# Optimization experiments

Measured on AMD Instinct MI355X. Metric: run time of the kernel, lower is better.

The kernel has to match this reference:

```python
import jax, jax.numpy as jnp
import numpy as np

N_NODES = 100000
N_EDGES = 1600000
D = 128
LAYERS = 3
LN_EPS = 1e-5


def setup_inputs() -> dict:
    key = jax.random.key(0)
    k1, k2, k3 = jax.random.split(key, 3)
    x = jax.random.normal(k1, (N_NODES, D), dtype=jnp.float32)
    edge_index = jax.random.randint(k2, (2, N_EDGES), 0, N_NODES, dtype=jnp.int64)
    W = jax.random.normal(k3, (LAYERS, D, D), dtype=jnp.float32) * (1.0 / np.sqrt(D))
    b = jnp.zeros((LAYERS, D), dtype=jnp.float32)
    ln_w = jnp.ones((LAYERS, D), dtype=jnp.float32)
    ln_b = jnp.zeros((LAYERS, D), dtype=jnp.float32)
    return {"x": x, "edge_index": edge_index, "W": W, "b": b, "ln_w": ln_w, "ln_b": ln_b}


def _gcn_conv(x, row, col, deg_inv_sqrt, W, b):
    # x: [N, D]; row/col: [E+N] (self-loops appended); PyG GCNConv math:
    # h = (D^-1/2 (A+I) D^-1/2) (x @ W) + b
    xw = x @ W  # [N, D]
    norm = deg_inv_sqrt[row] * deg_inv_sqrt[col]  # [E+N]
    msg = xw[row] * norm[:, None]  # gather + scale, memory-bound
    out = jax.ops.segment_sum(msg, col, num_segments=x.shape[0])  # scatter-add at targets
    return out + b


def _layer_norm(h, w, bset):
    mu = jnp.mean(h, axis=-1, keepdims=True)
    var = jnp.mean(jnp.square(h - mu), axis=-1, keepdims=True)
    return (h - mu) * jax.lax.rsqrt(var + LN_EPS) * w + bset


def reference(x, edge_index, W, b, ln_w, ln_b):
    n = x.shape[0]
    loops = jnp.arange(n, dtype=edge_index.dtype)
    row = jnp.concatenate([edge_index[0], loops])  # sources
    col = jnpp = jnp.concatenate([edge_index[1], loops])  # targets
    deg = jax.ops.segment_sum(jnp.ones_like(col, dtype=x.dtype), col, num_segments=n)
    deg_inv_sqrt = jax.lax.rsqrt(deg)  # deg >= 1 due to self-loops
    for i in range(LAYERS):
        h = _gcn_conv(x, row, col, deg_inv_sqrt, W[i], b[i])
        h = jax.nn.relu(h)
        h = h + x  # residual (shapes always match: in == emb)
        # dropout is identity in eval mode
        x = _layer_norm(h, ln_w[i], ln_b[i])
    return x
```

## Files before the change

kernel.cpp:

```cpp
#include <hip/hip_runtime.h>
#include <stdint.h>

#define NN 100000
#define NE 1600000
#define DD 128
#define NLAYERS 3
#define NB 196
#define BRS 9
#define NBLK 256
#define EPB 6250
#define CAP 96
#define ENTCAP 9216
#define OVFCAP 4096

typedef __attribute__((ext_vector_type(8))) short bf16x8;
typedef __attribute__((ext_vector_type(4))) float f32x4;
typedef __attribute__((ext_vector_type(4))) unsigned int u32x4;
typedef __attribute__((ext_vector_type(2))) unsigned int u32x2;
typedef __attribute__((ext_vector_type(2))) float f32x2;

__device__ __forceinline__ float bflo(uint32_t v){ return __uint_as_float(v << 16); }
__device__ __forceinline__ float bfhi(uint32_t v){ return __uint_as_float(v & 0xFFFF0000u); }
__device__ __forceinline__ float bf1(unsigned short u){ return __uint_as_float(((uint32_t)u) << 16); }
__device__ __forceinline__ unsigned short f2bf(float f){
  uint32_t u = __float_as_uint(f);
  u += 0x7FFFu + ((u >> 16) & 1u);
  return (unsigned short)(u >> 16);
}
__device__ __forceinline__ int colof(int j){ return ((j & 7) << 4) | (j >> 3); }

__global__ __launch_bounds__(256) void k_detect(const uint32_t* __restrict__ x,
                                                const uint32_t* __restrict__ ei,
                                                int* __restrict__ flags){
  __shared__ int s_f32, s_i32;
  if (threadIdx.x == 0){ s_f32 = 0; s_i32 = 0; }
  __syncthreads();
  int f = 0, i32 = 0;
  for (int idx = threadIdx.x; idx < 8192; idx += 256){
    uint32_t u = x[idx];
    if (((u >> 7) & 0xFFu) >= 0x90u) f++;
  }
  for (int idx = threadIdx.x; idx < 2048; idx += 256){
    if (ei[2*idx + 1] != 0u) i32++;
  }
  atomicAdd(&s_f32, f); atomicAdd(&s_i32, i32);
  __syncthreads();
  if (threadIdx.x == 0){
    flags[0] = (s_f32 > 100) ? 1 : 0;
    flags[1] = (s_i32 > 10) ? 0 : 1;
  }
}

__device__ __forceinline__ int load_edge(const int* ei, int i64m, size_t idx){
  if (i64m) return (int)((const uint32_t*)ei)[2*idx];
  return ei[idx];
}


__global__ __launch_bounds__(256) void k_params(const void* __restrict__ W, const void* __restrict__ b,
                                                const void* __restrict__ lnw, const void* __restrict__ lnb,
                                                const int* __restrict__ flags,
                                                unsigned short* __restrict__ wt,
                                                float* __restrict__ pbP, float* __restrict__ plwP,
                                                float* __restrict__ plbP){
  int l = blockIdx.x;
  int f32m = flags[0];
  for (int idx = threadIdx.x; idx < DD*DD; idx += 256){
    int k = idx >> 7, c = idx & 127;
    unsigned short v = f32m ? f2bf(((const float*)W)[l*DD*DD + idx])
                            : ((const unsigned short*)W)[l*DD*DD + idx];
    wt[l*DD*DD + c*DD + k] = v;
  }
  for (int idx = threadIdx.x; idx < DD; idx += 256){
    int c = colof(idx);
    if (f32m){
      pbP [l*DD+idx] = ((const float*)b)[l*DD+c];
      plwP[l*DD+idx] = ((const float*)lnw)[l*DD+c];
      plbP[l*DD+idx] = ((const float*)lnb)[l*DD+c];
    } else {
      pbP [l*DD+idx] = bf1(((const unsigned short*)b)[l*DD+c]);
      plwP[l*DD+idx] = bf1(((const unsigned short*)lnw)[l*DD+c]);
      plbP[l*DD+idx] = bf1(((const unsigned short*)lnb)[l*DD+c]);
    }
  }
}

__global__ __launch_bounds__(256) void k_cvt(const void* __restrict__ x, const int* __restrict__ flags,
                                             unsigned short* __restrict__ xb){
  size_t idx = (size_t)blockIdx.x*256 + threadIdx.x;
  size_t base = idx*8;
  if (base >= (size_t)NN*DD) return;
  if (flags[0]){
    const f32x4* xf = (const f32x4*)((const float*)x + base);
    f32x4 v0 = xf[0], v1 = xf[1];
    u32x4 o;
    o[0] = (uint32_t)f2bf(v0[0]) | ((uint32_t)f2bf(v0[1]) << 16);
    o[1] = (uint32_t)f2bf(v0[2]) | ((uint32_t)f2bf(v0[3]) << 16);
    o[2] = (uint32_t)f2bf(v1[0]) | ((uint32_t)f2bf(v1[1]) << 16);
    o[3] = (uint32_t)f2bf(v1[2]) | ((uint32_t)f2bf(v1[3]) << 16);
    *(u32x4*)(xb + base) = o;
  } else {
    *(u32x4*)(xb + base) = *(const u32x4*)((const unsigned short*)x + base);
  }
}

__global__ __launch_bounds__(256) void k_cells(const int* __restrict__ ei, const int* __restrict__ flags,
                                               uint32_t* __restrict__ cells, int* __restrict__ cellcnt,
                                               uint64_t* __restrict__ ovf, int* __restrict__ ovf_cnt){
  __shared__ int cnt[NB];
  int tid = threadIdx.x, blk = blockIdx.x;
  for (int b = tid; b < NB; b += 256) cnt[b] = 0;
  __syncthreads();
  int i64m = flags[1];
  int e0 = blk*EPB;
  for (int e = e0 + tid; e < e0 + EPB; e += 256){
    int c = load_edge(ei, i64m, (size_t)NE + e);
    if (c < 0) c = 0; if (c > NN-1) c = NN-1;
    int r = load_edge(ei, i64m, (size_t)e);
    if (r < 0) r = 0; if (r > NN-1) r = NN-1;
    int b = c >> BRS;
    uint32_t pack = ((uint32_t)r << BRS) | (uint32_t)(c & 511);
    int pos = atomicAdd(&cnt[b], 1);
    if (pos < CAP){
      cells[((size_t)blk*NB + b)*CAP + pos] = pack;
    } else {
      int op = atomicAdd(ovf_cnt, 1);
      if (op < OVFCAP) ovf[op] = ((uint64_t)b << 32) | (uint64_t)pack;
    }
  }
  __syncthreads();
  for (int b = tid; b < NB; b += 256){
    int v = cnt[b]; if (v > CAP) v = CAP;
    cellcnt[blk*NB + b] = v;
  }
}

__global__ __launch_bounds__(256) void k_btotal(const int* __restrict__ cellcnt,
                                                const uint64_t* __restrict__ ovf,
                                                const int* __restrict__ ovf_cnt,
                                                int* __restrict__ btot){
  int b = blockIdx.x, tid = threadIdx.x;
  int s = 0;
  for (int blk = tid; blk < NBLK; blk += 256) s += cellcnt[blk*NB + b];
  int oc = *ovf_cnt; if (oc > OVFCAP) oc = OVFCAP;
  for (int i = tid; i < oc; i += 256) if ((int)(ovf[i] >> 32) == b) s++;
  #pragma unroll
  for (int m = 1; m < 64; m <<= 1) s += __shfl_xor(s, m, 64);
  __shared__ int sm[4];
  int wid = tid >> 6, lane = tid & 63;
  if (lane == 0) sm[wid] = s;
  __syncthreads();
  if (tid == 0) btot[b] = sm[0] + sm[1] + sm[2] + sm[3];
}

__global__ __launch_bounds__(256) void k_bscan(const int* __restrict__ btot,
                                               int* __restrict__ bbase, int* __restrict__ colptr){
  __shared__ int sm[256];
  int tid = threadIdx.x;
  int v = (tid < NB) ? btot[tid] : 0;
  sm[tid] = v; __syncthreads();
  for (int o = 1; o < 256; o <<= 1){
    int t = (tid >= o) ? sm[tid - o] : 0;
    __syncthreads();
    sm[tid] += t;
    __syncthreads();
  }
  if (tid < NB) bbase[tid] = sm[tid] - v;
  if (tid == 0){
    int tot = sm[NB-1];
    bbase[NB] = tot;
    colptr[NN] = tot;
  }
}

__global__ __launch_bounds__(256) void k_csr(const uint32_t* __restrict__ cells,
                                             const int* __restrict__ cellcnt,
                                             const uint64_t* __restrict__ ovf,
                                             const int* __restrict__ ovf_cnt,
                                             const int* __restrict__ bbase,
                                             int* __restrict__ csr, int* __restrict__ colptr,
                                             float* __restrict__ dis){
  __shared__ uint32_t ent[ENTCAP];
  __shared__ int cnt2[512];
  __shared__ int off[512];
  __shared__ int m;
  int b = blockIdx.x, tid = threadIdx.x, lane = tid & 63, wid = tid >> 6;
  if (tid == 0) m = 0;
  for (int t = tid; t < 512; t += 256) cnt2[t] = 0;
  __syncthreads();
  {
    int blk = tid;
    int c = cellcnt[blk*NB + b];
    int base = atomicAdd(&m, c);
    const uint32_t* src = cells + ((size_t)blk*NB + b)*CAP;
    for (int k = 0; k < c; ++k){
      int p = base + k;
      if (p < ENTCAP) ent[p] = src[k];
    }
  }
  int oc = *ovf_cnt; if (oc > OVFCAP) oc = OVFCAP;
  for (int i = tid; i < oc; i += 256){
    uint64_t v = ovf[i];
    if ((int)(v >> 32) == b){
      int p = atomicAdd(&m, 1);
      if (p < ENTCAP) ent[p] = (uint32_t)v;
    }
  }
  __syncthreads();
  int mm = m; if (mm > ENTCAP) mm = ENTCAP;
  for (int i = tid; i < mm; i += 256) atomicAdd(&cnt2[ent[i] & 511], 1);
  __syncthreads();
  if (wid == 0){
    int loc[8]; int s = 0;
    #pragma unroll
    for (int k = 0; k < 8; ++k){ loc[k] = cnt2[lane*8 + k]; s += loc[k]; }
    int pref = s;
    #pragma unroll
    for (int d = 1; d < 64; d <<= 1){
      int t = __shfl_up(pref, d, 64);
      if (lane >= d) pref += t;
    }
    int run = pref - s;
    #pragma unroll
    for (int k = 0; k < 8; ++k){ off[lane*8 + k] = run; run += loc[k]; }
  }
  __syncthreads();
  int nbase = b << BRS;
  int gb = bbase[b];
  for (int t = tid; t < 512; t += 256){
    int node = nbase + t;
    if (node < NN){
      colptr[node] = gb + off[t];
      dis[node] = rsqrtf(1.0f + (float)cnt2[t]);
    }
  }
  __syncthreads();
  for (int i = tid; i < mm; i += 256){
    uint32_t e = ent[i];
    int t = e & 511;
    int pos = atomicAdd(&off[t], 1);
    csr[gb + pos] = (int)(e >> BRS);
  }
}


__global__ __launch_bounds__(256) void k_gemm(const unsigned short* __restrict__ x,
                                              const unsigned short* __restrict__ wt,
                                              const float* __restrict__ dis,
                                              int8_t* __restrict__ yq,
                                              float* __restrict__ qscale){
  int wave = threadIdx.x >> 6, lane = threadIdx.x & 63;
  int lr = lane & 15, lk = lane >> 4;
  int r0 = blockIdx.x*64 + wave*16;
  int arow = r0 + lr; if (arow > NN-1) arow = NN-1;

  f32x4 zero = {0.f, 0.f, 0.f, 0.f};
  f32x4 acc[8];
  #pragma unroll
  for (int cf = 0; cf < 8; ++cf) acc[cf] = zero;

  const bf16x8* xp = (const bf16x8*)(x + (size_t)arow*DD + lk*8);
  #pragma unroll
  for (int ks = 0; ks < 4; ++ks){
    bf16x8 a = xp[ks*4];
    #pragma unroll
    for (int cf = 0; cf < 8; ++cf){
      const bf16x8* wp = (const bf16x8*)(wt + (size_t)(cf*16 + lr)*DD + lk*8);
      bf16x8 bfr = wp[ks*4];
      acc[cf] = __builtin_amdgcn_mfma_f32_16x16x32_bf16(a, bfr, acc[cf], 0, 0, 0);
    }
  }

  #pragma unroll
  for (int t = 0; t < 4; ++t){
    int rr = r0 + lk*4 + t;
    float mx = 0.f;
    #pragma unroll
    for (int cf = 0; cf < 8; ++cf) mx = fmaxf(mx, fabsf(acc[cf][t]));
    #pragma unroll
    for (int m = 1; m < 16; m <<= 1) mx = fmaxf(mx, __shfl_xor(mx, m, 64));
    mx = fmaxf(mx, 1e-20f);
    float inv = 127.0f / mx;
    int q[8];
    #pragma unroll
    for (int cf = 0; cf < 8; ++cf){
      float v = fminf(fmaxf(acc[cf][t]*inv, -127.f), 127.f);
      q[cf] = (int)rintf(v);
    }
    uint32_t lo = (q[0] & 255) | ((q[1] & 255) << 8) | ((q[2] & 255) << 16) | ((q[3] & 255) << 24);
    uint32_t hi = (q[4] & 255) | ((q[5] & 255) << 8) | ((q[6] & 255) << 16) | ((q[7] & 255) << 24);
    if (rr < NN){
      u32x2 pk; pk[0] = lo; pk[1] = hi;
      *(u32x2*)(yq + (size_t)rr*DD + lr*8) = pk;
      if (lr == 0) qscale[rr] = (mx * (1.0f/127.0f)) * dis[rr];
    }
  }
}

__global__ __launch_bounds__(256) void k_agg(const int8_t* __restrict__ yq,
                                             const float* __restrict__ qscale,
                                             unsigned short* __restrict__ xb,
                                             void* __restrict__ out, int last,
                                             const int* __restrict__ flags,
                                             const int* __restrict__ colptr,
                                             const int* __restrict__ csr,
                                             const float* __restrict__ dis,
                                             const float* __restrict__ bbP,
                                             const float* __restrict__ lnwP,
                                             const float* __restrict__ lnbP){
  int wid = threadIdx.x >> 6, L = threadIdx.x & 63;
  int i = blockIdx.x*4 + wid;
  int s = colptr[i], e = colptr[i+1];
  s = __builtin_amdgcn_readfirstlane(s);
  e = __builtin_amdgcn_readfirstlane(e);
  int j2 = L*2;
  int c0 = 32*(L & 3) + (L >> 2), c1 = c0 + 16;

  float a0, a1;
  {
    float qs = qscale[i];
    uint16_t us = *(const uint16_t*)(yq + (size_t)i*DD + j2);
    a0 = qs * (float)(int)(int8_t)(us & 0xFF);
    a1 = qs * (float)(int)(int8_t)(us >> 8);
  }

  int j = s;
  for (; j + 8 <= e; j += 8){
    uint16_t us[8]; float qs[8];
    #pragma unroll
    for (int k = 0; k < 8; ++k){
      int src = csr[j+k];
      qs[k] = qscale[src];
      us[k] = *(const uint16_t*)(yq + (size_t)src*DD + j2);
    }
    #pragma unroll
    for (int k = 0; k < 8; ++k){
      a0 += qs[k] * (float)(int)(int8_t)(us[k] & 0xFF);
      a1 += qs[k] * (float)(int)(int8_t)(us[k] >> 8);
    }
  }
  for (; j < e; ++j){
    int src = csr[j];
    float qs = qscale[src];
    uint16_t us = *(const uint16_t*)(yq + (size_t)src*DD + j2);
    a0 += qs * (float)(int)(int8_t)(us & 0xFF);
    a1 += qs * (float)(int)(int8_t)(us >> 8);
  }

  float di = dis[i];
  f32x2 bv  = *(const f32x2*)(bbP  + j2);
  float h0 = fmaxf(a0*di + bv[0], 0.f);
  float h1 = fmaxf(a1*di + bv[1], 0.f);
  h0 += bf1(xb[(size_t)i*DD + c0]);
  h1 += bf1(xb[(size_t)i*DD + c1]);

  float s1 = h0 + h1, s2 = h0*h0 + h1*h1;
  #pragma unroll
  for (int m = 1; m < 64; m <<= 1){
    s1 += __shfl_xor(s1, m, 64);
    s2 += __shfl_xor(s2, m, 64);
  }
  float mean = s1*(1.f/128.f);
  float var  = s2*(1.f/128.f) - mean*mean;
  float rstd = rsqrtf(var + 1e-5f);
  f32x2 wv = *(const f32x2*)(lnwP + j2);
  f32x2 ov = *(const f32x2*)(lnbP + j2);
  float o0 = (h0 - mean)*rstd*wv[0] + ov[0];
  float o1 = (h1 - mean)*rstd*wv[1] + ov[1];
  if (!last){
    xb[(size_t)i*DD + c0] = f2bf(o0);
    xb[(size_t)i*DD + c1] = f2bf(o1);
  } else {
    if (flags[0]){
      float* of = (float*)out + (size_t)i*DD;
      of[c0] = o0; of[c1] = o1;
    } else {
      unsigned short* ob = (unsigned short*)out + (size_t)i*DD;
      ob[c0] = f2bf(o0); ob[c1] = f2bf(o1);
    }
  }
}


extern "C" void kernel_launch(void* const* d_in, const int* in_sizes, int n_in,
                              void* d_out, int out_size, void* d_ws, size_t ws_size,
                              hipStream_t stream){
  const void* x0  = d_in[0];
  const int*  ei  = (const int*)d_in[1];
  const void* W   = d_in[2];
  const void* b   = d_in[3];
  const void* lnw = d_in[4];
  const void* lnb = d_in[5];

  char* ws = (char*)d_ws;
  size_t off = 0;
  auto alloc = [&](size_t bytes)->char*{
    char* p = ws + off;
    off += (bytes + 255) & ~(size_t)255;
    return p;
  };
  unsigned short* xb = (unsigned short*)alloc((size_t)NN*DD*2);
  char* regionA = ws + off;
  int8_t* yq     = (int8_t*)alloc((size_t)NN*DD);
  float* qscale  = (float*)alloc((size_t)NN*4);
  unsigned short* wt = (unsigned short*)alloc((size_t)NLAYERS*DD*DD*2);
  float* pbP  = (float*)alloc((size_t)NLAYERS*DD*4);
  float* plwP = (float*)alloc((size_t)NLAYERS*DD*4);
  float* plbP = (float*)alloc((size_t)NLAYERS*DD*4);
  size_t cellsBytes = (size_t)NBLK*NB*CAP*4;
  size_t usedA = (size_t)(ws + off - regionA);
  if (usedA < cellsBytes) off += cellsBytes - usedA;
  uint32_t* cells = (uint32_t*)regionA;
  int* csr    = (int*)alloc((size_t)NE*4);
  int* colptr = (int*)alloc((size_t)(NN+1)*4);
  float* dis  = (float*)alloc((size_t)NN*4);
  int* cellcnt = (int*)alloc((size_t)NBLK*NB*4);
  int* btot    = (int*)alloc(NB*4);
  int* bbase   = (int*)alloc((NB+1)*4);
  uint64_t* ovf = (uint64_t*)alloc(OVFCAP*8);
  int* ovf_cnt  = (int*)alloc(256);
  int* flags = (int*)alloc(256);

  hipMemsetAsync(ovf_cnt, 0, 4, stream);

  k_detect<<<1, 256, 0, stream>>>((const uint32_t*)x0, (const uint32_t*)ei, flags);
  k_cvt<<<(NN*DD/8 + 255)/256, 256, 0, stream>>>(x0, flags, xb);
  k_cells<<<NBLK, 256, 0, stream>>>(ei, flags, cells, cellcnt, ovf, ovf_cnt);
  k_btotal<<<NB, 256, 0, stream>>>(cellcnt, ovf, ovf_cnt, btot);
  k_bscan<<<1, 256, 0, stream>>>(btot, bbase, colptr);
  k_csr<<<NB, 256, 0, stream>>>(cells, cellcnt, ovf, ovf_cnt, bbase, csr, colptr, dis);
  k_params<<<NLAYERS, 256, 0, stream>>>(W, b, lnw, lnb, flags, wt, pbP, plwP, plbP);

  for (int l = 0; l < NLAYERS; ++l){
    k_gemm<<<(NN + 63)/64, 256, 0, stream>>>(xb, wt + (size_t)l*DD*DD, dis, yq, qscale);
    k_agg<<<NN/4, 256, 0, stream>>>(yq, qscale, xb, d_out, (l == NLAYERS-1) ? 1 : 0, flags,
                                    colptr, csr, dis,
                                    pbP + (size_t)l*DD, plwP + (size_t)l*DD, plbP + (size_t)l*DD);
  }
}
```

Before: 391.6 us.

## Permute feature layout so aggregation uses 32 lanes per node with dword gathers

Hidden features and weights are stored in a permuted column order, so the GEMM's quantized output is contiguous in the order the aggregation consumes. Aggregation now gives each node half a wavefront (32 lanes), and each lane gathers a 4-byte int8 chunk instead of 2 bytes, which halves the number of gather instructions per edge. Edges are unrolled by 16, then 4, then 1. The aim is better memory-request efficiency in the gather-bound aggregation. The cost is that the final output must scatter through the permutation, and the per-node loop bounds are no longer wave-uniform.

New measurement: 384.6 us. Within noise of the previous version (-1.8%).

```diff
diff --git a/kernel.cpp b/kernel.cpp
--- a/kernel.cpp
+++ b/kernel.cpp
@@ -17,7 +17,6 @@
 typedef __attribute__((ext_vector_type(4))) float f32x4;
 typedef __attribute__((ext_vector_type(4))) unsigned int u32x4;
 typedef __attribute__((ext_vector_type(2))) unsigned int u32x2;
-typedef __attribute__((ext_vector_type(2))) float f32x2;
 
 __device__ __forceinline__ float bflo(uint32_t v){ return __uint_as_float(v << 16); }
 __device__ __forceinline__ float bfhi(uint32_t v){ return __uint_as_float(v & 0xFFFF0000u); }
@@ -28,6 +27,9 @@
   return (unsigned short)(u >> 16);
 }
 __device__ __forceinline__ int colof(int j){ return ((j & 7) << 4) | (j >> 3); }
+__device__ __forceinline__ float b2f(uint32_t d, int t){
+  return (float)(int)(int8_t)(d >> (8*t));
+}
 
 __global__ __launch_bounds__(256) void k_detect(const uint32_t* __restrict__ x,
                                                 const uint32_t* __restrict__ ei,
@@ -60,16 +62,17 @@
 __global__ __launch_bounds__(256) void k_params(const void* __restrict__ W, const void* __restrict__ b,
                                                 const void* __restrict__ lnw, const void* __restrict__ lnb,
                                                 const int* __restrict__ flags,
-                                                unsigned short* __restrict__ wt,
+                                                unsigned short* __restrict__ wtP,
                                                 float* __restrict__ pbP, float* __restrict__ plwP,
                                                 float* __restrict__ plbP){
   int l = blockIdx.x;
   int f32m = flags[0];
   for (int idx = threadIdx.x; idx < DD*DD; idx += 256){
-    int k = idx >> 7, c = idx & 127;
-    unsigned short v = f32m ? f2bf(((const float*)W)[l*DD*DD + idx])
-                            : ((const unsigned short*)W)[l*DD*DD + idx];
-    wt[l*DD*DD + c*DD + k] = v;
+    int c = idx >> 7, j = idx & 127;
+    int src = colof(j)*DD + c;
+    unsigned short v = f32m ? f2bf(((const float*)W)[l*DD*DD + src])
+                            : ((const unsigned short*)W)[l*DD*DD + src];
+    wtP[l*DD*DD + idx] = v;
   }
   for (int idx = threadIdx.x; idx < DD; idx += 256){
     int c = colof(idx);
@@ -86,22 +89,27 @@
 }
 
 __global__ __launch_bounds__(256) void k_cvt(const void* __restrict__ x, const int* __restrict__ flags,
-                                             unsigned short* __restrict__ xb){
+                                             unsigned short* __restrict__ xbP){
   size_t idx = (size_t)blockIdx.x*256 + threadIdx.x;
   size_t base = idx*8;
   if (base >= (size_t)NN*DD) return;
+  int i = (int)(base >> 7), j0 = (int)(base & 127);
+  unsigned short v[8];
   if (flags[0]){
-    const f32x4* xf = (const f32x4*)((const float*)x + base);
-    f32x4 v0 = xf[0], v1 = xf[1];
-    u32x4 o;
-    o[0] = (uint32_t)f2bf(v0[0]) | ((uint32_t)f2bf(v0[1]) << 16);
-    o[1] = (uint32_t)f2bf(v0[2]) | ((uint32_t)f2bf(v0[3]) << 16);
-    o[2] = (uint32_t)f2bf(v1[0]) | ((uint32_t)f2bf(v1[1]) << 16);
-    o[3] = (uint32_t)f2bf(v1[2]) | ((uint32_t)f2bf(v1[3]) << 16);
-    *(u32x4*)(xb + base) = o;
+    const float* xf = (const float*)x + (size_t)i*DD;
+    #pragma unroll
+    for (int t = 0; t < 8; ++t) v[t] = f2bf(xf[colof(j0+t)]);
   } else {
-    *(u32x4*)(xb + base) = *(const u32x4*)((const unsigned short*)x + base);
-  }
+    const unsigned short* xs = (const unsigned short*)x + (size_t)i*DD;
+    #pragma unroll
+    for (int t = 0; t < 8; ++t) v[t] = xs[colof(j0+t)];
+  }
+  u32x4 o;
+  o[0] = (uint32_t)v[0] | ((uint32_t)v[1] << 16);
+  o[1] = (uint32_t)v[2] | ((uint32_t)v[3] << 16);
+  o[2] = (uint32_t)v[4] | ((uint32_t)v[5] << 16);
+  o[3] = (uint32_t)v[6] | ((uint32_t)v[7] << 16);
+  *(u32x4*)(xbP + base) = o;
 }
 
 __global__ __launch_bounds__(256) void k_cells(const int* __restrict__ ei, const int* __restrict__ flags,
@@ -299,7 +307,7 @@
 
 __global__ __launch_bounds__(256) void k_agg(const int8_t* __restrict__ yq,
                                              const float* __restrict__ qscale,
-                                             unsigned short* __restrict__ xb,
+                                             unsigned short* __restrict__ xbP,
                                              void* __restrict__ out, int last,
                                              const int* __restrict__ flags,
                                              const int* __restrict__ colptr,
@@ -308,75 +316,103 @@
                                              const float* __restrict__ bbP,
                                              const float* __restrict__ lnwP,
                                              const float* __restrict__ lnbP){
-  int wid = threadIdx.x >> 6, L = threadIdx.x & 63;
-  int i = blockIdx.x*4 + wid;
+  int wid = threadIdx.x >> 6;
+  int half = (threadIdx.x >> 5) & 1;
+  int hl = threadIdx.x & 31;
+  int i = blockIdx.x*8 + wid*2 + half;
+  const uint32_t* yq4 = (const uint32_t*)yq;
+
   int s = colptr[i], e = colptr[i+1];
-  s = __builtin_amdgcn_readfirstlane(s);
-  e = __builtin_amdgcn_readfirstlane(e);
-  int j2 = L*2;
-  int c0 = 32*(L & 3) + (L >> 2), c1 = c0 + 16;
-
-  float a0, a1;
+  float a0, a1, a2, a3;
   {
     float qs = qscale[i];
-    uint16_t us = *(const uint16_t*)(yq + (size_t)i*DD + j2);
-    a0 = qs * (float)(int)(int8_t)(us & 0xFF);
-    a1 = qs * (float)(int)(int8_t)(us >> 8);
+    uint32_t d = yq4[((uint32_t)i << 5) + hl];
+    a0 = qs*b2f(d,0); a1 = qs*b2f(d,1); a2 = qs*b2f(d,2); a3 = qs*b2f(d,3);
   }
 
   int j = s;
-  for (; j + 8 <= e; j += 8){
-    uint16_t us[8]; float qs[8];
-    #pragma unroll
-    for (int k = 0; k < 8; ++k){
-      int src = csr[j+k];
-      qs[k] = qscale[src];
-      us[k] = *(const uint16_t*)(yq + (size_t)src*DD + j2);
-    }
-    #pragma unroll
-    for (int k = 0; k < 8; ++k){
-      a0 += qs[k] * (float)(int)(int8_t)(us[k] & 0xFF);
-      a1 += qs[k] * (float)(int)(int8_t)(us[k] >> 8);
-    }
-  }
-  for (; j < e; ++j){
+  while (j + 16 <= e){
+    int sr[16]; float qs[16]; uint32_t dv[16];
+    #pragma unroll
+    for (int k = 0; k < 16; ++k) sr[k] = csr[j+k];
+    #pragma unroll
+    for (int k = 0; k < 16; ++k){
+      qs[k] = qscale[sr[k]];
+      dv[k] = yq4[((uint32_t)sr[k] << 5) + hl];
+    }
+    #pragma unroll
+    for (int k = 0; k < 16; ++k){
+      a0 += qs[k]*b2f(dv[k],0); a1 += qs[k]*b2f(dv[k],1);
+      a2 += qs[k]*b2f(dv[k],2); a3 += qs[k]*b2f(dv[k],3);
+    }
+    j += 16;
+  }
+  while (j + 4 <= e){
+    int sr[4]; float qs[4]; uint32_t dv[4];
+    #pragma unroll
+    for (int k = 0; k < 4; ++k) sr[k] = csr[j+k];
+    #pragma unroll
+    for (int k = 0; k < 4; ++k){
+      qs[k] = qscale[sr[k]];
+      dv[k] = yq4[((uint32_t)sr[k] << 5) + hl];
+    }
+    #pragma unroll
+    for (int k = 0; k < 4; ++k){
+      a0 += qs[k]*b2f(dv[k],0); a1 += qs[k]*b2f(dv[k],1);
+      a2 += qs[k]*b2f(dv[k],2); a3 += qs[k]*b2f(dv[k],3);
+    }
+    j += 4;
+  }
+  while (j < e){
     int src = csr[j];
     float qs = qscale[src];
-    uint16_t us = *(const uint16_t*)(yq + (size_t)src*DD + j2);
-    a0 += qs * (float)(int)(int8_t)(us & 0xFF);
-    a1 += qs * (float)(int)(int8_t)(us >> 8);
+    uint32_t d = yq4[((uint32_t)src << 5) + hl];
+    a0 += qs*b2f(d,0); a1 += qs*b2f(d,1); a2 += qs*b2f(d,2); a3 += qs*b2f(d,3);
+    ++j;
   }
 
   float di = dis[i];
-  f32x2 bv  = *(const f32x2*)(bbP  + j2);
+  f32x4 bv = *(const f32x4*)(bbP + 4*hl);
   float h0 = fmaxf(a0*di + bv[0], 0.f);
   float h1 = fmaxf(a1*di + bv[1], 0.f);
-  h0 += bf1(xb[(size_t)i*DD + c0]);
-  h1 += bf1(xb[(size_t)i*DD + c1]);
-
-  float s1 = h0 + h1, s2 = h0*h0 + h1*h1;
+  float h2 = fmaxf(a2*di + bv[2], 0.f);
+  float h3 = fmaxf(a3*di + bv[3], 0.f);
+  u32x2 xv = *(const u32x2*)(xbP + (size_t)i*DD + 4*hl);
+  h0 += bflo(xv[0]); h1 += bfhi(xv[0]);
+  h2 += bflo(xv[1]); h3 += bfhi(xv[1]);
+
+  float s1 = h0 + h1 + h2 + h3;
+  float s2 = h0*h0 + h1*h1 + h2*h2 + h3*h3;
   #pragma unroll
-  for (int m = 1; m < 64; m <<= 1){
+  for (int m = 1; m < 32; m <<= 1){
     s1 += __shfl_xor(s1, m, 64);
     s2 += __shfl_xor(s2, m, 64);
   }
   float mean = s1*(1.f/128.f);
   float var  = s2*(1.f/128.f) - mean*mean;
   float rstd = rsqrtf(var + 1e-5f);
-  f32x2 wv = *(const f32x2*)(lnwP + j2);
-  f32x2 ov = *(const f32x2*)(lnbP + j2);
+  f32x4 wv = *(const f32x4*)(lnwP + 4*hl);
+  f32x4 ov = *(const f32x4*)(lnbP + 4*hl);
   float o0 = (h0 - mean)*rstd*wv[0] + ov[0];
   float o1 = (h1 - mean)*rstd*wv[1] + ov[1];
+  float o2 = (h2 - mean)*rstd*wv[2] + ov[2];
+  float o3 = (h3 - mean)*rstd*wv[3] + ov[3];
+
   if (!last){
-    xb[(size_t)i*DD + c0] = f2bf(o0);
-    xb[(size_t)i*DD + c1] = f2bf(o1);
+    u32x2 pk;
+    pk[0] = (uint32_t)f2bf(o0) | ((uint32_t)f2bf(o1) << 16);
+    pk[1] = (uint32_t)f2bf(o2) | ((uint32_t)f2bf(o3) << 16);
+    *(u32x2*)(xbP + (size_t)i*DD + 4*hl) = pk;
   } else {
+    float o[4] = {o0, o1, o2, o3};
     if (flags[0]){
       float* of = (float*)out + (size_t)i*DD;
-      of[c0] = o0; of[c1] = o1;
+      #pragma unroll
+      for (int t = 0; t < 4; ++t) of[colof(4*hl + t)] = o[t];
     } else {
       unsigned short* ob = (unsigned short*)out + (size_t)i*DD;
-      ob[c0] = f2bf(o0); ob[c1] = f2bf(o1);
+      #pragma unroll
+      for (int t = 0; t < 4; ++t) ob[colof(4*hl + t)] = f2bf(o[t]);
     }
   }
 }
@@ -399,11 +435,11 @@
     off += (bytes + 255) & ~(size_t)255;
     return p;
   };
-  unsigned short* xb = (unsigned short*)alloc((size_t)NN*DD*2);
+  unsigned short* xbP = (unsigned short*)alloc((size_t)NN*DD*2);
   char* regionA = ws + off;
   int8_t* yq     = (int8_t*)alloc((size_t)NN*DD);
   float* qscale  = (float*)alloc((size_t)NN*4);
-  unsigned short* wt = (unsigned short*)alloc((size_t)NLAYERS*DD*DD*2);
+  unsigned short* wtP = (unsigned short*)alloc((size_t)NLAYERS*DD*DD*2);
   float* pbP  = (float*)alloc((size_t)NLAYERS*DD*4);
   float* plwP = (float*)alloc((size_t)NLAYERS*DD*4);
   float* plbP = (float*)alloc((size_t)NLAYERS*DD*4);
@@ -424,16 +460,16 @@
   hipMemsetAsync(ovf_cnt, 0, 4, stream);
 
   k_detect<<<1, 256, 0, stream>>>((const uint32_t*)x0, (const uint32_t*)ei, flags);
-  k_cvt<<<(NN*DD/8 + 255)/256, 256, 0, stream>>>(x0, flags, xb);
+  k_cvt<<<(NN*DD/8 + 255)/256, 256, 0, stream>>>(x0, flags, xbP);
   k_cells<<<NBLK, 256, 0, stream>>>(ei, flags, cells, cellcnt, ovf, ovf_cnt);
   k_btotal<<<NB, 256, 0, stream>>>(cellcnt, ovf, ovf_cnt, btot);
   k_bscan<<<1, 256, 0, stream>>>(btot, bbase, colptr);
   k_csr<<<NB, 256, 0, stream>>>(cells, cellcnt, ovf, ovf_cnt, bbase, csr, colptr, dis);
-  k_params<<<NLAYERS, 256, 0, stream>>>(W, b, lnw, lnb, flags, wt, pbP, plwP, plbP);
+  k_params<<<NLAYERS, 256, 0, stream>>>(W, b, lnw, lnb, flags, wtP, pbP, plwP, plbP);
 
   for (int l = 0; l < NLAYERS; ++l){
-    k_gemm<<<(NN + 63)/64, 256, 0, stream>>>(xb, wt + (size_t)l*DD*DD, dis, yq, qscale);
-    k_agg<<<NN/4, 256, 0, stream>>>(yq, qscale, xb, d_out, (l == NLAYERS-1) ? 1 : 0, flags,
+    k_gemm<<<(NN + 63)/64, 256, 0, stream>>>(xbP, wtP + (size_t)l*DD*DD, dis, yq, qscale);
+    k_agg<<<NN/8, 256, 0, stream>>>(yq, qscale, xbP, d_out, (l == NLAYERS-1) ? 1 : 0, flags,
                                     colptr, csr, dis,
                                     pbP + (size_t)l*DD, plwP + (size_t)l*DD, plbP + (size_t)l*DD);
   }
```
